# Performance work log

Measured on AMD Instinct MI355X. Metric: run time of the kernel, lower is better.

The kernel has to match this reference:

```python
import jax, jax.numpy as jnp
import numpy as np

N = 100000      # nodes
E = 1600000     # edges (avg degree 16)
DIN, DH, DOUT = 128, 128, 64


def setup_inputs() -> dict:
    key = jax.random.key(0)
    k0, k1, k2, k3 = jax.random.split(key, 4)
    x = jax.random.normal(k0, (N, DIN), jnp.float32)
    edge_index = jax.random.randint(k1, (2, E), 0, N, dtype=jnp.int64)
    W1 = jax.random.normal(k2, (DIN, DH), jnp.float32) / np.sqrt(DIN).astype(np.float32)
    b1 = jnp.zeros((DH,), jnp.float32)
    W2 = jax.random.normal(k3, (DH, DOUT), jnp.float32) / np.sqrt(DH).astype(np.float32)
    b2 = jnp.zeros((DOUT,), jnp.float32)
    return {"x": x, "edge_index": edge_index, "W1": W1, "b1": b1, "W2": W2, "b2": b2}


def reference(x, edge_index, W1, b1, W2, b2):
    n = x.shape[0]
    # PyG GCNConv: add self-loops, symmetric normalization deg^-1/2 A_hat deg^-1/2
    loops = jnp.arange(n, dtype=edge_index.dtype)
    src = jnp.concatenate([edge_index[0], loops])  # message sources
    dst = jnp.concatenate([edge_index[1], loops])  # aggregation targets
    deg = jax.ops.segment_sum(jnp.ones(src.shape, x.dtype), dst, num_segments=n)
    dinv = jnp.where(deg > 0, jax.lax.rsqrt(deg), 0.0)
    norm = dinv[src] * dinv[dst]                    # [E+N]

    def gcn_conv(h, W, b):
        h = h @ W                                   # dense transform first (PyG order)
        msg = h[src] * norm[:, None]                # gather + scale
        return jax.ops.segment_sum(msg, dst, num_segments=n) + b

    h = jax.nn.relu(gcn_conv(x, W1, b1))
    # F.dropout is identity in eval mode (self.training == False)
    return gcn_conv(h, W2, b2)
```

## Files before the change

kernel.cpp:

```cpp
#include <hip/hip_runtime.h>

#define DIN 128
#define DH  128
#define DOUT 64

typedef __attribute__((ext_vector_type(8))) short bf16x8;
typedef __attribute__((ext_vector_type(4))) float f32x4;


__device__ inline unsigned bf16rne(float f) {
    unsigned u = __float_as_uint(f);
    return (u + 0x7fffu + ((u >> 16) & 1u)) >> 16;
}

__device__ inline void acc8(float* a, uint4 v) {
    a[0] += __uint_as_float(v.x << 16); a[1] += __uint_as_float(v.x & 0xffff0000u);
    a[2] += __uint_as_float(v.y << 16); a[3] += __uint_as_float(v.y & 0xffff0000u);
    a[4] += __uint_as_float(v.z << 16); a[5] += __uint_as_float(v.z & 0xffff0000u);
    a[6] += __uint_as_float(v.w << 16); a[7] += __uint_as_float(v.w & 0xffff0000u);
}


__global__ void k_count_rank(const int* __restrict__ dst, int* __restrict__ cnt,
                             int* __restrict__ rank, int E, int pad) {
    int e = blockIdx.x * 256 + threadIdx.x;
    if (e < E) rank[e] = atomicAdd(&cnt[dst[e] * pad], 1);
}

__global__ void k_dinv(const int* __restrict__ cnt, float* __restrict__ dinv, int n, int pad) {
    int i = blockIdx.x * 256 + threadIdx.x;
    if (i < n) dinv[i] = rsqrtf((float)(cnt[i * pad] + 1));
}

__global__ void k_scan_partial(const int* __restrict__ cnt, int* __restrict__ excl,
                               int* __restrict__ bsum, int n, int pad) {
    __shared__ int sd[256];
    int t = threadIdx.x;
    int base = blockIdx.x * 1024 + t * 4;
    int v0 = (base + 0 < n) ? cnt[(base + 0) * pad] : 0;
    int v1 = (base + 1 < n) ? cnt[(base + 1) * pad] : 0;
    int v2 = (base + 2 < n) ? cnt[(base + 2) * pad] : 0;
    int v3 = (base + 3 < n) ? cnt[(base + 3) * pad] : 0;
    int s = v0 + v1 + v2 + v3;
    sd[t] = s;
    __syncthreads();
    for (int off = 1; off < 256; off <<= 1) {
        int x = (t >= off) ? sd[t - off] : 0;
        __syncthreads();
        sd[t] += x;
        __syncthreads();
    }
    int incl = sd[t];
    if (t == 255) bsum[blockIdx.x] = incl;
    int run = incl - s;
    if (base + 0 < n) excl[base + 0] = run;  run += v0;
    if (base + 1 < n) excl[base + 1] = run;  run += v1;
    if (base + 2 < n) excl[base + 2] = run;  run += v2;
    if (base + 3 < n) excl[base + 3] = run;
}

__global__ void k_scan_bsum(int* __restrict__ bsum, int nb) {
    __shared__ int sd[256];
    int t = threadIdx.x;
    int v = (t < nb) ? bsum[t] : 0;
    sd[t] = v;
    __syncthreads();
    for (int off = 1; off < 256; off <<= 1) {
        int x = (t >= off) ? sd[t - off] : 0;
        __syncthreads();
        sd[t] += x;
        __syncthreads();
    }
    if (t < nb) bsum[t] = sd[t] - v;
}

__global__ void k_finalize(int* __restrict__ rowstart, const int* __restrict__ bsum,
                           int n, int E) {
    int i = blockIdx.x * 256 + threadIdx.x;
    if (i < n) rowstart[i] += bsum[i >> 10];
    if (i == 0) rowstart[n] = E;
}

__global__ void k_fill2(const int* __restrict__ src, const int* __restrict__ dst,
                        const int* __restrict__ rank, const int* __restrict__ rowstart,
                        int* __restrict__ adj, int E) {
    int e = blockIdx.x * 256 + threadIdx.x;
    if (e < E) adj[rowstart[dst[e]] + rank[e]] = src[e];
}


__global__ void k_wsplit_frag(const float* __restrict__ W, unsigned short* __restrict__ Wf_hi,
                              unsigned short* __restrict__ Wf_lo, int N) {
    int idx = blockIdx.x * 256 + threadIdx.x;
    if (idx >= N * 128) return;
    int f = idx >> 9;
    int r = idx & 511;
    int lane = r >> 3;
    int j = r & 7;
    int t = f >> 2;
    int ks = f & 3;
    int n = t * 16 + (lane & 15);
    int k = ks * 32 + (lane >> 4) * 8 + j;
    float v = W[(size_t)k * N + n];
    unsigned h = bf16rne(v);
    float hf = __uint_as_float(h << 16);
    unsigned l = bf16rne(v - hf);
    Wf_hi[idx] = (unsigned short)h;
    Wf_lo[idx] = (unsigned short)l;
}


template <int NCOLS>
__global__ __launch_bounds__(256, 2) void k_gemm_mfma(
        const float* __restrict__ A,
        const unsigned short* __restrict__ Wf_hi,
        const unsigned short* __restrict__ Wf_lo,
        const float* __restrict__ dinv,
        unsigned short* __restrict__ S, int M, int nchunks) {
    constexpr int NT = NCOLS / 16;
    constexpr int NFRAG = NT * 4;
    __shared__ unsigned short lh[NFRAG * 512];
    __shared__ unsigned short ll[NFRAG * 512];
    int tid = threadIdx.x;
    constexpr int NV = NFRAG * 512 * 2 / 16;
    #pragma unroll
    for (int i = 0; i < NV / 256; i++) {
        int s = tid + i * 256;
        ((uint4*)lh)[s] = ((const uint4*)Wf_hi)[s];
        ((uint4*)ll)[s] = ((const uint4*)Wf_lo)[s];
    }
    __syncthreads();

    int wave = tid >> 6;
    int lane = tid & 63;
    int kfrag = (lane >> 4) * 8;
    int bcol = lane & 15;
    const unsigned short* lhp = lh + lane * 8;
    const unsigned short* llp = ll + lane * 8;

    for (int chunk = blockIdx.x; chunk < nchunks; chunk += gridDim.x) {
        int row0 = chunk * 64 + wave * 16;
        int arow = row0 + (lane & 15);
        if (arow >= M) arow = M - 1;
        const float* ap = A + (size_t)arow * 128 + kfrag;

        float4 av[4][2];
        #pragma unroll
        for (int ks = 0; ks < 4; ks++) {
            av[ks][0] = *(const float4*)(ap + ks * 32);
            av[ks][1] = *(const float4*)(ap + ks * 32 + 4);
        }

        f32x4 acc[NT];
        #pragma unroll
        for (int t = 0; t < NT; t++) acc[t] = (f32x4){0.f, 0.f, 0.f, 0.f};

        #pragma unroll
        for (int ks = 0; ks < 4; ks++) {
            float a8[8] = {av[ks][0].x, av[ks][0].y, av[ks][0].z, av[ks][0].w,
                           av[ks][1].x, av[ks][1].y, av[ks][1].z, av[ks][1].w};
            bf16x8 ahi, alo;
            #pragma unroll
            for (int j = 0; j < 8; j++) {
                unsigned h = bf16rne(a8[j]);
                float hf = __uint_as_float(h << 16);
                ahi[j] = (short)h;
                alo[j] = (short)bf16rne(a8[j] - hf);
            }
            #pragma unroll
            for (int t = 0; t < NT; t++) {
                int f = t * 4 + ks;
                bf16x8 bhi = *(const bf16x8*)(lhp + f * 512);
                bf16x8 blo = *(const bf16x8*)(llp + f * 512);
                acc[t] = __builtin_amdgcn_mfma_f32_16x16x32_bf16(ahi, bhi, acc[t], 0, 0, 0);
                acc[t] = __builtin_amdgcn_mfma_f32_16x16x32_bf16(ahi, blo, acc[t], 0, 0, 0);
                acc[t] = __builtin_amdgcn_mfma_f32_16x16x32_bf16(alo, bhi, acc[t], 0, 0, 0);
            }
        }

        int srow0 = row0 + (lane >> 4) * 4;
        #pragma unroll
        for (int r = 0; r < 4; r++) {
            int row = srow0 + r;
            float dv = (row < M) ? dinv[row] : 0.f;
            #pragma unroll
            for (int t = 0; t < NT; t++) {
                unsigned o = bf16rne(dv * acc[t][r]);
                unsigned p = (unsigned)__shfl_xor((int)o, 1);
                if ((lane & 1) == 0 && row < M)
                    *(unsigned*)(S + (size_t)row * NCOLS + t * 16 + bcol) = o | (p << 16);
            }
        }
    }
}


template <bool RELU>
__global__ void k_agg128(const unsigned short* __restrict__ S, const int* __restrict__ rowstart,
                         const int* __restrict__ adj, const float* __restrict__ dinv,
                         const float* __restrict__ bias, float* __restrict__ out, int n) {
    int wave = threadIdx.x >> 6;
    int lane = threadIdx.x & 63;
    int node = blockIdx.x * 4 + wave;
    if (node >= n) return;
    int start = rowstart[node];
    int end   = rowstart[node + 1];
    int g  = lane >> 4;
    int fo = lane & 15;

    const uint4* S4 = (const uint4*)S;
    float a0[8] = {}, a1[8] = {};

    while (start < end) {
        int cnt = end - start;
        if (cnt > 64) cnt = 64;
        int nb = adj[start + (lane < cnt ? lane : cnt - 1)];
        int t = 0;
        for (; t + 16 <= cnt; t += 16) {
            int jA = __shfl(nb, t + 0  + g);
            int jB = __shfl(nb, t + 4  + g);
            int jC = __shfl(nb, t + 8  + g);
            int jD = __shfl(nb, t + 12 + g);
            uint4 mA = S4[(size_t)jA * 16 + fo];
            uint4 mB = S4[(size_t)jB * 16 + fo];
            uint4 mC = S4[(size_t)jC * 16 + fo];
            uint4 mD = S4[(size_t)jD * 16 + fo];
            acc8(a0, mA); acc8(a1, mB); acc8(a0, mC); acc8(a1, mD);
        }
        for (; t + 4 <= cnt; t += 4) {
            int j = __shfl(nb, t + g);
            uint4 m = S4[(size_t)j * 16 + fo];
            acc8(a0, m);
        }
        if (t < cnt) {
            int i1 = t + g;
            int j = __shfl(nb, i1 < cnt ? i1 : cnt - 1);
            uint4 m = S4[(size_t)j * 16 + fo];
            if (i1 < cnt) acc8(a1, m);
        }
        start += 64;
    }

    float acc[8];
    #pragma unroll
    for (int i = 0; i < 8; i++) {
        float v = a0[i] + a1[i];
        v += __shfl_xor(v, 16);
        v += __shfl_xor(v, 32);
        acc[i] = v;
    }

    uint4 selfu = ((const uint4*)S)[(size_t)node * 16 + fo];
    float self[8] = {};
    acc8(self, selfu);
    float dv = dinv[node];
    float4 bb0 = ((const float4*)bias)[fo * 2 + 0];
    float4 bb1 = ((const float4*)bias)[fo * 2 + 1];
    float o[8];
    o[0] = dv * (acc[0] + self[0]) + bb0.x;
    o[1] = dv * (acc[1] + self[1]) + bb0.y;
    o[2] = dv * (acc[2] + self[2]) + bb0.z;
    o[3] = dv * (acc[3] + self[3]) + bb0.w;
    o[4] = dv * (acc[4] + self[4]) + bb1.x;
    o[5] = dv * (acc[5] + self[5]) + bb1.y;
    o[6] = dv * (acc[6] + self[6]) + bb1.z;
    o[7] = dv * (acc[7] + self[7]) + bb1.w;
    if (RELU) {
        #pragma unroll
        for (int i = 0; i < 8; i++) o[i] = fmaxf(o[i], 0.f);
    }
    if (g == 0) {
        float4* op = (float4*)(out + (size_t)node * 128 + fo * 8);
        op[0] = make_float4(o[0], o[1], o[2], o[3]);
        op[1] = make_float4(o[4], o[5], o[6], o[7]);
    }
}

__global__ void k_agg64(const unsigned short* __restrict__ S, const int* __restrict__ rowstart,
                        const int* __restrict__ adj, const float* __restrict__ dinv,
                        const float* __restrict__ bias, float* __restrict__ out, int n) {
    int wave = threadIdx.x >> 6;
    int lane = threadIdx.x & 63;
    int node = blockIdx.x * 4 + wave;
    if (node >= n) return;
    int start = rowstart[node];
    int end   = rowstart[node + 1];
    int g  = lane >> 3;
    int fo = lane & 7;

    const uint4* S4 = (const uint4*)S;
    float a0[8] = {}, a1[8] = {};

    while (start < end) {
        int cnt = end - start;
        if (cnt > 64) cnt = 64;
        int nb = adj[start + (lane < cnt ? lane : cnt - 1)];
        int t = 0;
        for (; t + 32 <= cnt; t += 32) {
            int jA = __shfl(nb, t + 0  + g);
            int jB = __shfl(nb, t + 8  + g);
            int jC = __shfl(nb, t + 16 + g);
            int jD = __shfl(nb, t + 24 + g);
            uint4 mA = S4[(size_t)jA * 8 + fo];
            uint4 mB = S4[(size_t)jB * 8 + fo];
            uint4 mC = S4[(size_t)jC * 8 + fo];
            uint4 mD = S4[(size_t)jD * 8 + fo];
            acc8(a0, mA); acc8(a1, mB); acc8(a0, mC); acc8(a1, mD);
        }
        for (; t + 8 <= cnt; t += 8) {
            int j = __shfl(nb, t + g);
            uint4 m = S4[(size_t)j * 8 + fo];
            acc8(a0, m);
        }
        if (t < cnt) {
            int i1 = t + g;
            int j = __shfl(nb, i1 < cnt ? i1 : cnt - 1);
            uint4 m = S4[(size_t)j * 8 + fo];
            if (i1 < cnt) acc8(a1, m);
        }
        start += 64;
    }

    float acc[8];
    #pragma unroll
    for (int i = 0; i < 8; i++) {
        float v = a0[i] + a1[i];
        v += __shfl_xor(v, 8);
        v += __shfl_xor(v, 16);
        v += __shfl_xor(v, 32);
        acc[i] = v;
    }

    uint4 selfu = ((const uint4*)S)[(size_t)node * 8 + fo];
    float self[8] = {};
    acc8(self, selfu);
    float dv = dinv[node];
    float4 bb0 = ((const float4*)bias)[fo * 2 + 0];
    float4 bb1 = ((const float4*)bias)[fo * 2 + 1];
    float o[8];
    o[0] = dv * (acc[0] + self[0]) + bb0.x;
    o[1] = dv * (acc[1] + self[1]) + bb0.y;
    o[2] = dv * (acc[2] + self[2]) + bb0.z;
    o[3] = dv * (acc[3] + self[3]) + bb0.w;
    o[4] = dv * (acc[4] + self[4]) + bb1.x;
    o[5] = dv * (acc[5] + self[5]) + bb1.y;
    o[6] = dv * (acc[6] + self[6]) + bb1.z;
    o[7] = dv * (acc[7] + self[7]) + bb1.w;
    if (g == 0) {
        float4* op = (float4*)(out + (size_t)node * 64 + fo * 8);
        op[0] = make_float4(o[0], o[1], o[2], o[3]);
        op[1] = make_float4(o[4], o[5], o[6], o[7]);
    }
}


extern "C" void kernel_launch(void* const* d_in, const int* in_sizes, int n_in,
                              void* d_out, int out_size, void* d_ws, size_t ws_size,
                              hipStream_t stream) {
    const float* x  = (const float*)d_in[0];
    const int*   ei = (const int*)d_in[1];
    const float* W1 = (const float*)d_in[2];
    const float* b1 = (const float*)d_in[3];
    const float* W2 = (const float*)d_in[4];
    const float* b2 = (const float*)d_in[5];
    float* out = (float*)d_out;

    int N = in_sizes[0] / DIN;
    int E = in_sizes[1] / 2;
    const int* esrc = ei;
    const int* edst = ei + E;

    size_t fixed = (size_t)N * 128 * 2
                 + (size_t)N * 128 * 4
                 + (size_t)N * 4
                 + (size_t)(N + 1) * 4
                 + (size_t)E * 4 * 2
                 + (128 + 64) * 128 * 2 * 2
                 + 1024 * 4 + 16 * 256;
    int PAD = (fixed + (size_t)N * 16 * 4 <= ws_size) ? 16 : 1;

    char* wsb = (char*)d_ws;
    size_t off = 0;
    auto alloc = [&](size_t bytes) {
        void* p = wsb + off;
        off = (off + bytes + 255) & ~(size_t)255;
        return p;
    };
    unsigned short* S = (unsigned short*)alloc((size_t)N * 128 * 2);
    float* H1       = (float*)alloc((size_t)N * 128 * 4);
    float* dinv     = (float*)alloc((size_t)N * 4);
    int*   rowstart = (int*)alloc((size_t)(N + 1) * 4);
    int*   adj      = (int*)alloc((size_t)E * 4);
    int*   rank     = (int*)alloc((size_t)E * 4);
    unsigned short* wf1h = (unsigned short*)alloc(128 * 128 * 2);
    unsigned short* wf1l = (unsigned short*)alloc(128 * 128 * 2);
    unsigned short* wf2h = (unsigned short*)alloc(64 * 128 * 2);
    unsigned short* wf2l = (unsigned short*)alloc(64 * 128 * 2);
    int*   cnt      = (int*)alloc((size_t)N * PAD * 4);
    int*   bsum     = (int*)alloc(1024 * 4);

    int eb = (E + 255) / 256;
    int nb = (N + 255) / 256;
    int sb = (N + 1023) / 1024;

    k_wsplit_frag<<<(128 * 128) / 256, 256, 0, stream>>>(W1, wf1h, wf1l, 128);
    k_wsplit_frag<<<(64 * 128) / 256, 256, 0, stream>>>(W2, wf2h, wf2l, 64);

    hipMemsetAsync(cnt, 0, (size_t)N * PAD * 4, stream);
    k_count_rank<<<eb, 256, 0, stream>>>(edst, cnt, rank, E, PAD);
    k_dinv<<<nb, 256, 0, stream>>>(cnt, dinv, N, PAD);
    k_scan_partial<<<sb, 256, 0, stream>>>(cnt, rowstart, bsum, N, PAD);
    k_scan_bsum<<<1, 256, 0, stream>>>(bsum, sb);
    k_finalize<<<nb, 256, 0, stream>>>(rowstart, bsum, N, E);
    k_fill2<<<eb, 256, 0, stream>>>(esrc, edst, rank, rowstart, adj, E);

    int nchunks = (N + 63) / 64;
    int gb = nchunks < 512 ? nchunks : 512;
    int ab = (N + 3) / 4;

    k_gemm_mfma<128><<<gb, 256, 0, stream>>>(x, wf1h, wf1l, dinv, S, N, nchunks);
    k_agg128<true><<<ab, 256, 0, stream>>>(S, rowstart, adj, dinv, b1, H1, N);

    k_gemm_mfma<64><<<gb, 256, 0, stream>>>(H1, wf2h, wf2l, dinv, S, N, nchunks);
    k_agg64<<<ab, 256, 0, stream>>>(S, rowstart, adj, dinv, b2, out, N);
}
```

Baseline: 279.8 us.

## Split GEMM output columns across wave pairs with 512-thread blocks

The MFMA transform kernel now runs 512-thread blocks in which each pair of waves shares a 16-row group and each wave computes half the output column tiles. This halves the accumulator registers per wave and doubles the waves available to hide latency. The cost is that both waves in a pair load and split the same A rows, which duplicates global reads and conversion work. The packed 32-bit shuffle store is also replaced by plain 16-bit stores, dropping the shuffle but issuing narrower writes.

```diff
diff --git a/kernel.cpp b/kernel.cpp
--- a/kernel.cpp
+++ b/kernel.cpp
@@ -111,35 +111,36 @@
 
 
 template <int NCOLS>
-__global__ __launch_bounds__(256, 2) void k_gemm_mfma(
+__global__ __launch_bounds__(512, 4) void k_gemm_mfma(
         const float* __restrict__ A,
         const unsigned short* __restrict__ Wf_hi,
         const unsigned short* __restrict__ Wf_lo,
         const float* __restrict__ dinv,
         unsigned short* __restrict__ S, int M, int nchunks) {
     constexpr int NT = NCOLS / 16;
+    constexpr int NTW = NT / 2;
     constexpr int NFRAG = NT * 4;
     __shared__ unsigned short lh[NFRAG * 512];
     __shared__ unsigned short ll[NFRAG * 512];
     int tid = threadIdx.x;
-    constexpr int NV = NFRAG * 512 * 2 / 16;
-    #pragma unroll
-    for (int i = 0; i < NV / 256; i++) {
-        int s = tid + i * 256;
-        ((uint4*)lh)[s] = ((const uint4*)Wf_hi)[s];
-        ((uint4*)ll)[s] = ((const uint4*)Wf_lo)[s];
+    constexpr int NV4 = NFRAG * 64;
+    for (int i = tid; i < NV4; i += 512) {
+        ((uint4*)lh)[i] = ((const uint4*)Wf_hi)[i];
+        ((uint4*)ll)[i] = ((const uint4*)Wf_lo)[i];
     }
     __syncthreads();
 
     int wave = tid >> 6;
     int lane = tid & 63;
+    int rowg = wave >> 1;
+    int colh = wave & 1;
     int kfrag = (lane >> 4) * 8;
     int bcol = lane & 15;
     const unsigned short* lhp = lh + lane * 8;
     const unsigned short* llp = ll + lane * 8;
 
     for (int chunk = blockIdx.x; chunk < nchunks; chunk += gridDim.x) {
-        int row0 = chunk * 64 + wave * 16;
+        int row0 = chunk * 64 + rowg * 16;
         int arow = row0 + (lane & 15);
         if (arow >= M) arow = M - 1;
         const float* ap = A + (size_t)arow * 128 + kfrag;
@@ -151,9 +152,9 @@
             av[ks][1] = *(const float4*)(ap + ks * 32 + 4);
         }
 
-        f32x4 acc[NT];
+        f32x4 acc[NTW];
         #pragma unroll
-        for (int t = 0; t < NT; t++) acc[t] = (f32x4){0.f, 0.f, 0.f, 0.f};
+        for (int t = 0; t < NTW; t++) acc[t] = (f32x4){0.f, 0.f, 0.f, 0.f};
 
         #pragma unroll
         for (int ks = 0; ks < 4; ks++) {
@@ -168,8 +169,8 @@
                 alo[j] = (short)bf16rne(a8[j] - hf);
             }
             #pragma unroll
-            for (int t = 0; t < NT; t++) {
-                int f = t * 4 + ks;
+            for (int t = 0; t < NTW; t++) {
+                int f = (colh * NTW + t) * 4 + ks;
                 bf16x8 bhi = *(const bf16x8*)(lhp + f * 512);
                 bf16x8 blo = *(const bf16x8*)(llp + f * 512);
                 acc[t] = __builtin_amdgcn_mfma_f32_16x16x32_bf16(ahi, bhi, acc[t], 0, 0, 0);
@@ -184,11 +185,10 @@
             int row = srow0 + r;
             float dv = (row < M) ? dinv[row] : 0.f;
             #pragma unroll
-            for (int t = 0; t < NT; t++) {
+            for (int t = 0; t < NTW; t++) {
                 unsigned o = bf16rne(dv * acc[t][r]);
-                unsigned p = (unsigned)__shfl_xor((int)o, 1);
-                if ((lane & 1) == 0 && row < M)
-                    *(unsigned*)(S + (size_t)row * NCOLS + t * 16 + bcol) = o | (p << 16);
+                if (row < M)
+                    S[(size_t)row * NCOLS + (colh * NTW + t) * 16 + bcol] = (unsigned short)o;
             }
         }
     }
@@ -418,9 +418,9 @@
     int gb = nchunks < 512 ? nchunks : 512;
     int ab = (N + 3) / 4;
 
-    k_gemm_mfma<128><<<gb, 256, 0, stream>>>(x, wf1h, wf1l, dinv, S, N, nchunks);
+    k_gemm_mfma<128><<<gb, 512, 0, stream>>>(x, wf1h, wf1l, dinv, S, N, nchunks);
     k_agg128<true><<<ab, 256, 0, stream>>>(S, rowstart, adj, dinv, b1, H1, N);
 
-    k_gemm_mfma<64><<<gb, 256, 0, stream>>>(H1, wf2h, wf2l, dinv, S, N, nchunks);
+    k_gemm_mfma<64><<<gb, 512, 0, stream>>>(H1, wf2h, wf2l, dinv, S, N, nchunks);
     k_agg64<<<ab, 256, 0, stream>>>(S, rowstart, adj, dinv, b2, out, N);
 }
```

Result: slower. 299.8 us (+7.1%).

## Read GEMM weight fragments from global memory and launch one block per chunk

Applied to the files above, without the earlier changes.

The GEMM kernel no longer stages the hi/lo bf16 weight fragments in shared memory behind a barrier. Each wave now reads them straight from global memory, relying on L1/L2 caching. The persistent grid-stride loop is replaced by one block per 64-row chunk, and the next K-slice of A is prefetched while the current one is multiplied. Launch bounds go up to 4 blocks per SM. This removes the LDS staging cost and the sync, but adds repeated global and cache reads of the weights in the MFMA loop.

```diff
diff --git a/kernel.cpp b/kernel.cpp
--- a/kernel.cpp
+++ b/kernel.cpp
@@ -111,85 +111,68 @@
 
 
 template <int NCOLS>
-__global__ __launch_bounds__(256, 2) void k_gemm_mfma(
+__global__ __launch_bounds__(256, 4) void k_gemm_mfma(
         const float* __restrict__ A,
-        const unsigned short* __restrict__ Wf_hi,
-        const unsigned short* __restrict__ Wf_lo,
+        const unsigned short* __restrict__ Bh,
+        const unsigned short* __restrict__ Bl,
         const float* __restrict__ dinv,
-        unsigned short* __restrict__ S, int M, int nchunks) {
+        unsigned short* __restrict__ S, int M) {
     constexpr int NT = NCOLS / 16;
-    constexpr int NFRAG = NT * 4;
-    __shared__ unsigned short lh[NFRAG * 512];
-    __shared__ unsigned short ll[NFRAG * 512];
-    int tid = threadIdx.x;
-    constexpr int NV = NFRAG * 512 * 2 / 16;
+    int wave = threadIdx.x >> 6;
+    int lane = threadIdx.x & 63;
+    int row0 = blockIdx.x * 64 + wave * 16;
+    int arow = row0 + (lane & 15);
+    if (arow >= M) arow = M - 1;
+    const float* ap = A + (size_t)arow * 128 + (lane >> 4) * 8;
+    const unsigned short* bhp = Bh + lane * 8;
+    const unsigned short* blp = Bl + lane * 8;
+
+    float4 a0 = *(const float4*)(ap);
+    float4 a1 = *(const float4*)(ap + 4);
+
+    f32x4 acc[NT];
     #pragma unroll
-    for (int i = 0; i < NV / 256; i++) {
-        int s = tid + i * 256;
-        ((uint4*)lh)[s] = ((const uint4*)Wf_hi)[s];
-        ((uint4*)ll)[s] = ((const uint4*)Wf_lo)[s];
-    }
-    __syncthreads();
-
-    int wave = tid >> 6;
-    int lane = tid & 63;
-    int kfrag = (lane >> 4) * 8;
+    for (int t = 0; t < NT; t++) acc[t] = (f32x4){0.f, 0.f, 0.f, 0.f};
+
+    #pragma unroll
+    for (int ks = 0; ks < 4; ks++) {
+        float4 n0, n1;
+        if (ks < 3) {
+            n0 = *(const float4*)(ap + (ks + 1) * 32);
+            n1 = *(const float4*)(ap + (ks + 1) * 32 + 4);
+        }
+        float a8[8] = {a0.x, a0.y, a0.z, a0.w, a1.x, a1.y, a1.z, a1.w};
+        bf16x8 ahi, alo;
+        #pragma unroll
+        for (int j = 0; j < 8; j++) {
+            unsigned h = bf16rne(a8[j]);
+            float hf = __uint_as_float(h << 16);
+            ahi[j] = (short)h;
+            alo[j] = (short)bf16rne(a8[j] - hf);
+        }
+        #pragma unroll
+        for (int t = 0; t < NT; t++) {
+            bf16x8 bh = *(const bf16x8*)(bhp + (size_t)(t * 4 + ks) * 512);
+            bf16x8 bl = *(const bf16x8*)(blp + (size_t)(t * 4 + ks) * 512);
+            acc[t] = __builtin_amdgcn_mfma_f32_16x16x32_bf16(ahi, bh, acc[t], 0, 0, 0);
+            acc[t] = __builtin_amdgcn_mfma_f32_16x16x32_bf16(ahi, bl, acc[t], 0, 0, 0);
+            acc[t] = __builtin_amdgcn_mfma_f32_16x16x32_bf16(alo, bh, acc[t], 0, 0, 0);
+        }
+        a0 = n0; a1 = n1;
+    }
+
+    int srow0 = row0 + (lane >> 4) * 4;
     int bcol = lane & 15;
-    const unsigned short* lhp = lh + lane * 8;
-    const unsigned short* llp = ll + lane * 8;
-
-    for (int chunk = blockIdx.x; chunk < nchunks; chunk += gridDim.x) {
-        int row0 = chunk * 64 + wave * 16;
-        int arow = row0 + (lane & 15);
-        if (arow >= M) arow = M - 1;
-        const float* ap = A + (size_t)arow * 128 + kfrag;
-
-        float4 av[4][2];
+    #pragma unroll
+    for (int r = 0; r < 4; r++) {
+        int row = srow0 + r;
+        float dv = (row < M) ? dinv[row] : 0.f;
         #pragma unroll
-        for (int ks = 0; ks < 4; ks++) {
-            av[ks][0] = *(const float4*)(ap + ks * 32);
-            av[ks][1] = *(const float4*)(ap + ks * 32 + 4);
-        }
-
-        f32x4 acc[NT];
-        #pragma unroll
-        for (int t = 0; t < NT; t++) acc[t] = (f32x4){0.f, 0.f, 0.f, 0.f};
-
-        #pragma unroll
-        for (int ks = 0; ks < 4; ks++) {
-            float a8[8] = {av[ks][0].x, av[ks][0].y, av[ks][0].z, av[ks][0].w,
-                           av[ks][1].x, av[ks][1].y, av[ks][1].z, av[ks][1].w};
-            bf16x8 ahi, alo;
-            #pragma unroll
-            for (int j = 0; j < 8; j++) {
-                unsigned h = bf16rne(a8[j]);
-                float hf = __uint_as_float(h << 16);
-                ahi[j] = (short)h;
-                alo[j] = (short)bf16rne(a8[j] - hf);
-            }
-            #pragma unroll
-            for (int t = 0; t < NT; t++) {
-                int f = t * 4 + ks;
-                bf16x8 bhi = *(const bf16x8*)(lhp + f * 512);
-                bf16x8 blo = *(const bf16x8*)(llp + f * 512);
-                acc[t] = __builtin_amdgcn_mfma_f32_16x16x32_bf16(ahi, bhi, acc[t], 0, 0, 0);
-                acc[t] = __builtin_amdgcn_mfma_f32_16x16x32_bf16(ahi, blo, acc[t], 0, 0, 0);
-                acc[t] = __builtin_amdgcn_mfma_f32_16x16x32_bf16(alo, bhi, acc[t], 0, 0, 0);
-            }
-        }
-
-        int srow0 = row0 + (lane >> 4) * 4;
-        #pragma unroll
-        for (int r = 0; r < 4; r++) {
-            int row = srow0 + r;
-            float dv = (row < M) ? dinv[row] : 0.f;
-            #pragma unroll
-            for (int t = 0; t < NT; t++) {
-                unsigned o = bf16rne(dv * acc[t][r]);
-                unsigned p = (unsigned)__shfl_xor((int)o, 1);
-                if ((lane & 1) == 0 && row < M)
-                    *(unsigned*)(S + (size_t)row * NCOLS + t * 16 + bcol) = o | (p << 16);
-            }
+        for (int t = 0; t < NT; t++) {
+            unsigned o = bf16rne(dv * acc[t][r]);
+            unsigned p = (unsigned)__shfl_xor((int)o, 1);
+            if ((lane & 1) == 0 && row < M)
+                *(unsigned*)(S + (size_t)row * NCOLS + t * 16 + bcol) = o | (p << 16);
         }
     }
 }
@@ -414,13 +397,12 @@
     k_finalize<<<nb, 256, 0, stream>>>(rowstart, bsum, N, E);
     k_fill2<<<eb, 256, 0, stream>>>(esrc, edst, rank, rowstart, adj, E);
 
-    int nchunks = (N + 63) / 64;
-    int gb = nchunks < 512 ? nchunks : 512;
+    int gb = (N + 63) / 64;
     int ab = (N + 3) / 4;
 
-    k_gemm_mfma<128><<<gb, 256, 0, stream>>>(x, wf1h, wf1l, dinv, S, N, nchunks);
+    k_gemm_mfma<128><<<gb, 256, 0, stream>>>(x, wf1h, wf1l, dinv, S, N);
     k_agg128<true><<<ab, 256, 0, stream>>>(S, rowstart, adj, dinv, b1, H1, N);
 
-    k_gemm_mfma<64><<<gb, 256, 0, stream>>>(H1, wf2h, wf2l, dinv, S, N, nchunks);
+    k_gemm_mfma<64><<<gb, 256, 0, stream>>>(H1, wf2h, wf2l, dinv, S, N);
     k_agg64<<<ab, 256, 0, stream>>>(S, rowstart, adj, dinv, b2, out, N);
 }
```

Measured after the change: 268.5 us. 1.04x faster.
